# Kernel optimization log

Measured on AMD Instinct MI355X. Metric: run time of the kernel, lower is better.

The kernel has to match this reference:

```python
import jax, jax.numpy as jnp
import numpy as np

N, D, C = 4096, 512, 64
MARGIN = 1.0
INF = jnp.float32(1e30)


def setup_inputs() -> dict:
    key = jax.random.key(0)
    k1, k2 = jax.random.split(key)
    embeddings = jax.random.normal(k1, (N, D), dtype=jnp.float32)
    targets = jax.random.randint(k2, (N,), 0, C)
    return {"embeddings": embeddings, "targets": targets}


def _triplet_loss(embeddings, targets, margin=MARGIN):
    # Squared pairwise distances [N, N] (differentiable, used for the loss)
    sq_norms = jnp.sum(embeddings * embeddings, axis=1)
    sq_dist = jnp.maximum(
        sq_norms[:, None] + sq_norms[None, :] - 2.0 * (embeddings @ embeddings.T), 0.0
    )
    # Euclidean distances for mining only (index selection is non-differentiable in torch)
    dist = jnp.sqrt(jax.lax.stop_gradient(sq_dist))

    same = targets[:, None] == targets[None, :]  # [N, N] same-label mask

    # Hardest negative per anchor: argmax_k (d_ap - d_ak + margin) == argmin_k d_ak over negatives
    neg_dist = jnp.where(same, INF, dist)
    n_idx = jnp.argmin(neg_dist, axis=1)   # [N] hardest negative index per anchor
    min_neg = jnp.min(neg_dist, axis=1)    # [N] its euclidean distance

    idx = jnp.arange(dist.shape[0])
    # anchor-positive pairs: same label, a < p (torch.combinations on sorted indices)
    pair_mask = same & (idx[:, None] < idx[None, :])
    # triplet kept only if mined loss (euclidean) strictly positive
    valid = pair_mask & (dist - min_neg[:, None] + margin > 0)

    ap_sq = sq_dist                         # [N, N] squared anchor-positive distances
    an_sq = sq_dist[idx, n_idx]             # [N]   squared anchor-hard-negative distances
    losses = jax.nn.relu(ap_sq - an_sq[:, None] + margin)

    cnt = jnp.sum(valid)
    denom = jnp.maximum(cnt, 1).astype(losses.dtype)
    loss = jnp.sum(jnp.where(valid, losses, 0.0)) / denom

    correct = jnp.sum(valid & (ap_sq < an_sq[:, None]))
    accuracy = correct.astype(jnp.float32) / jnp.maximum(cnt, 1).astype(jnp.float32)
    return loss, accuracy


def reference(embeddings, targets):
    return _triplet_loss(embeddings, targets)
```

## Files before the change

kernel.cpp:

```cpp
#include <hip/hip_runtime.h>

#define N 4096
#define D 512
#define C 64
#define MARGIN 1.0f
#define TILE 128
#define ROWB 128
#define NTILES (N / TILE)
#define NTRI (NTILES * (NTILES + 1) / 2)
#define FINF 3.0e38f
#define SLOTW 16
#define PCAP 1024
#define LOSSB 128

typedef __attribute__((ext_vector_type(8))) short short8;
typedef __attribute__((ext_vector_type(4))) float floatx4;

__device__ __forceinline__ unsigned short f2bf(float f) {
  unsigned int u = __float_as_uint(f);
  u += 0x7FFFu + ((u >> 16) & 1u);
  return (unsigned short)(u >> 16);
}

__device__ __forceinline__ void gload_lds16(const void* g, void* l) {
  __builtin_amdgcn_global_load_lds(
      (const __attribute__((address_space(1))) unsigned int*)g,
      (__attribute__((address_space(3))) unsigned int*)l, 16, 0, 0);
}

__global__ __launch_bounds__(256) void prep_kernel(const float* __restrict__ E,
                                                   unsigned short* __restrict__ Ebf,
                                                   float* __restrict__ norms,
                                                   unsigned int* __restrict__ an_sq_bits,
                                                   unsigned int* __restrict__ accs_u,
                                                   unsigned int* __restrict__ ctrl) {
  const int row = blockIdx.x;
  const int tid = threadIdx.x;
  if (row == N) {
    for (int k = tid; k < C * SLOTW; k += 256) accs_u[k] = 0u;
    if (tid < 2) ctrl[tid] = 0u;
    return;
  }
  if (row < 16) an_sq_bits[row * 256 + tid] = 0x7F800000u;
  const float2 v = reinterpret_cast<const float2*>(E + (size_t)row * D)[tid];
  float s = v.x * v.x + v.y * v.y;
  unsigned int packed = ((unsigned int)f2bf(v.y) << 16) | (unsigned int)f2bf(v.x);
  reinterpret_cast<unsigned int*>(Ebf + (size_t)row * D)[tid] = packed;
  for (int off = 32; off > 0; off >>= 1) s += __shfl_down(s, off);
  __shared__ float wsum[4];
  if ((tid & 63) == 0) wsum[tid >> 6] = s;
  __syncthreads();
  if (tid == 0) norms[row] = wsum[0] + wsum[1] + wsum[2] + wsum[3];
}

__global__ __launch_bounds__(256, 3) void gemm_min_kernel(const unsigned short* __restrict__ Ebf,
                                                          const float* __restrict__ norms,
                                                          const int* __restrict__ targets,
                                                          unsigned int* __restrict__ an_sq_bits,
                                                          uint2* __restrict__ pairs,
                                                          unsigned int* __restrict__ ctrl) {
  const int u = blockIdx.x;
  int i = (int)((sqrtf(8.0f * (float)u + 1.0f) - 1.0f) * 0.5f);
  while ((i + 1) * (i + 2) / 2 <= u) ++i;
  while (i * (i + 1) / 2 > u) --i;
  const int tm = u - i * (i + 1) / 2;
  const int tn = i;

  __shared__ alignas(16) unsigned char As[TILE * ROWB];
  __shared__ alignas(16) unsigned char Bs[TILE * ROWB];
  __shared__ float s_rmin[2][TILE];
  __shared__ float s_cmin[2][TILE];
  __shared__ unsigned int s_pkey[PCAP];
  __shared__ float s_psq[PCAP];
  __shared__ unsigned int s_pcnt, s_pbase;

  const int tid = threadIdx.x;
  const int wave = tid >> 6, lane = tid & 63;
  const int quad = lane >> 4, l16 = lane & 15;
  const int wr = wave >> 1, wc = wave & 1;
  const int rowBase = tm * TILE, colBase = tn * TILE;
  if (tid == 0) s_pcnt = 0u;

  const int lr = lane >> 3;
  const int lq = (lane & 7) ^ lr;
  const int lofs = lr * (D * 2) + lq * 16;
  const unsigned char* gA = (const unsigned char*)Ebf + (size_t)rowBase * (D * 2);
  const unsigned char* gB = (const unsigned char*)Ebf + (size_t)colBase * (D * 2);

  const int swz = l16 & 7;
  int rA[4], rB[4], cq[2];
#pragma unroll
  for (int s = 0; s < 4; s++) {
    rA[s] = (wr * 64 + s * 16 + l16) * ROWB;
    rB[s] = (wc * 64 + s * 16 + l16) * ROWB;
  }
#pragma unroll
  for (int ks = 0; ks < 2; ks++) cq[ks] = ((ks * 4 + quad) ^ swz) * 16;

  floatx4 acc[4][4];
#pragma unroll
  for (int a = 0; a < 4; a++)
#pragma unroll
    for (int b = 0; b < 4; b++) acc[a][b] = (floatx4){0.f, 0.f, 0.f, 0.f};

  for (int k0b = 0; k0b < D * 2; k0b += 128) {
#pragma unroll
    for (int t = 0; t < 4; t++) {
      const int g = wave * 4 + t;
      gload_lds16(gA + (size_t)g * 8 * (D * 2) + lofs + k0b, As + g * 1024);
      gload_lds16(gB + (size_t)g * 8 * (D * 2) + lofs + k0b, Bs + g * 1024);
    }
    __syncthreads();
#pragma unroll
    for (int ks = 0; ks < 2; ks++) {
      short8 af[4], bf[4];
#pragma unroll
      for (int s = 0; s < 4; s++) {
        af[s] = *reinterpret_cast<const short8*>(As + rA[s] + cq[ks]);
        bf[s] = *reinterpret_cast<const short8*>(Bs + rB[s] + cq[ks]);
      }
#pragma unroll
      for (int sm = 0; sm < 4; sm++)
#pragma unroll
        for (int sn = 0; sn < 4; sn++)
          acc[sm][sn] = __builtin_amdgcn_mfma_f32_16x16x32_bf16(af[sm], bf[sn], acc[sm][sn], 0, 0, 0);
    }
    __syncthreads();
  }

  int tcol[4], gcolv[4];
  float ncol[4];
#pragma unroll
  for (int sn = 0; sn < 4; sn++) {
    const int gc = colBase + wc * 64 + sn * 16 + l16;
    gcolv[sn] = gc;
    tcol[sn] = targets[gc];
    ncol[sn] = norms[gc];
  }
  float colmin[4] = {FINF, FINF, FINF, FINF};
#pragma unroll
  for (int sm = 0; sm < 4; sm++) {
#pragma unroll
    for (int r = 0; r < 4; r++) {
      const int rloc = wr * 64 + sm * 16 + quad * 4 + r;
      const int grow = rowBase + rloc;
      const int trow = targets[grow];
      const float nrow = norms[grow];
      float rowmin = FINF;
#pragma unroll
      for (int sn = 0; sn < 4; sn++) {
        const float sq = fmaxf(nrow + ncol[sn] - 2.0f * acc[sm][sn][r], 0.0f);
        if (tcol[sn] != trow) {
          rowmin = fminf(rowmin, sq);
          colmin[sn] = fminf(colmin[sn], sq);
        } else if (grow < gcolv[sn]) {
          const unsigned int idx = atomicAdd(&s_pcnt, 1u);
          if (idx < PCAP) {
            s_pkey[idx] = ((unsigned int)grow << 12) | (unsigned int)gcolv[sn];
            s_psq[idx] = sq;
          } else {
            const unsigned int g = atomicAdd(&ctrl[0], 1u);
            pairs[g] = make_uint2(((unsigned int)grow << 12) | (unsigned int)gcolv[sn],
                                  __float_as_uint(sq));
          }
        }
      }
#pragma unroll
      for (int off = 1; off < 16; off <<= 1) rowmin = fminf(rowmin, __shfl_xor(rowmin, off));
      if (l16 == 0) s_rmin[wc][rloc] = rowmin;
    }
  }
#pragma unroll
  for (int sn = 0; sn < 4; sn++) {
    float cm = colmin[sn];
    cm = fminf(cm, __shfl_xor(cm, 16));
    cm = fminf(cm, __shfl_xor(cm, 32));
    if (quad == 0) s_cmin[wr][wc * 64 + sn * 16 + l16] = cm;
  }
  __syncthreads();
  if (tid < TILE) {
    const float m = fminf(s_rmin[0][tid], s_rmin[1][tid]);
    if (m < FINF) atomicMin(&an_sq_bits[rowBase + tid], __float_as_uint(m));
  } else {
    const int c = tid - TILE;
    const float m = fminf(s_cmin[0][c], s_cmin[1][c]);
    if (m < FINF) atomicMin(&an_sq_bits[colBase + c], __float_as_uint(m));
  }
  const unsigned int npair = min(s_pcnt, (unsigned int)PCAP);
  if (tid == 0) s_pbase = atomicAdd(&ctrl[0], npair);
  __syncthreads();
  for (unsigned int r = tid; r < npair; r += 256)
    pairs[s_pbase + r] = make_uint2(s_pkey[r], __float_as_uint(s_psq[r]));
}

__global__ __launch_bounds__(256) void loss_kernel(const uint2* __restrict__ pairs,
                                                   const unsigned int* __restrict__ an_sq_bits,
                                                   float* __restrict__ accs,
                                                   unsigned int* __restrict__ ctrl,
                                                   float* __restrict__ out) {
  const int tid = threadIdx.x, wave = tid >> 6, lane = tid & 63;
  const unsigned int M = ctrl[0];
  __shared__ float s_sum[4];
  __shared__ unsigned int s_cnt[4], s_cor[4];
  __shared__ int s_last;
  float bsum = 0.f;
  unsigned int bcnt = 0, bcor = 0;
  for (unsigned int r = blockIdx.x * 256 + tid; r < M; r += LOSSB * 256) {
    const uint2 rec = pairs[r];
    const int a = (int)(rec.x >> 12);
    const float sq = __uint_as_float(rec.y);
    const float an = __uint_as_float(an_sq_bits[a]);
    if (sqrtf(sq) - sqrtf(an) + MARGIN > 0.0f) {
      bcnt++;
      bsum += fmaxf(sq - an + MARGIN, 0.0f);
      if (sq < an) bcor++;
    }
  }
#pragma unroll
  for (int off = 32; off > 0; off >>= 1) {
    bsum += __shfl_down(bsum, off);
    bcnt += __shfl_down(bcnt, off);
    bcor += __shfl_down(bcor, off);
  }
  if (lane == 0) { s_sum[wave] = bsum; s_cnt[wave] = bcnt; s_cor[wave] = bcor; }
  __syncthreads();
  if (tid == 0) {
    float* slot = accs + (size_t)(blockIdx.x & (C - 1)) * SLOTW;
    atomicAdd(&slot[0], s_sum[0] + s_sum[1] + s_sum[2] + s_sum[3]);
    atomicAdd((unsigned int*)&slot[1], s_cnt[0] + s_cnt[1] + s_cnt[2] + s_cnt[3]);
    atomicAdd((unsigned int*)&slot[2], s_cor[0] + s_cor[1] + s_cor[2] + s_cor[3]);
    __threadfence();
    s_last = (atomicAdd(&ctrl[1], 1u) == (unsigned int)LOSSB - 1u);
  }
  __syncthreads();
  if (s_last) {
    __threadfence();
    if (tid < C) {
      float sum = __uint_as_float(atomicAdd((unsigned int*)&accs[(size_t)tid * SLOTW + 0], 0u));
      unsigned int cnt = atomicAdd((unsigned int*)&accs[(size_t)tid * SLOTW + 1], 0u);
      unsigned int cor = atomicAdd((unsigned int*)&accs[(size_t)tid * SLOTW + 2], 0u);
#pragma unroll
      for (int off = 32; off > 0; off >>= 1) {
        sum += __shfl_down(sum, off);
        cnt += __shfl_down(cnt, off);
        cor += __shfl_down(cor, off);
      }
      if (tid == 0) {
        const float denom = (float)(cnt > 0u ? cnt : 1u);
        out[0] = sum / denom;
        out[1] = (float)cor / denom;
      }
    }
  }
}

extern "C" void kernel_launch(void* const* d_in, const int* in_sizes, int n_in,
                              void* d_out, int out_size, void* d_ws, size_t ws_size,
                              hipStream_t stream) {
  const float* E = (const float*)d_in[0];
  const int* targets = (const int*)d_in[1];
  float* out = (float*)d_out;
  char* ws = (char*)d_ws;
  size_t off = 0;
  unsigned short* Ebf = (unsigned short*)(ws + off); off += (size_t)N * D * 2;
  float* norms = (float*)(ws + off); off += (size_t)N * 4;
  unsigned int* an_sq = (unsigned int*)(ws + off); off += (size_t)N * 4;
  float* accs = (float*)(ws + off); off += (size_t)C * SLOTW * 4;
  unsigned int* ctrl = (unsigned int*)(ws + off); off += 256;
  uint2* pairs = (uint2*)(ws + off);

  prep_kernel<<<dim3(N + 1), dim3(256), 0, stream>>>(E, Ebf, norms, an_sq, (unsigned int*)accs, ctrl);
  gemm_min_kernel<<<dim3(NTRI), dim3(256), 0, stream>>>(Ebf, norms, targets, an_sq, pairs, ctrl);
  loss_kernel<<<dim3(LOSSB), dim3(256), 0, stream>>>(pairs, an_sq, accs, ctrl, out);
}
```

Baseline: 95.93 us.

## Fuse prep, GEMM-min and loss into one persistent kernel with grid barriers

Replaces the three kernel launches with a single persistent kernel of 512 blocks. Each block first converts rows to bf16 and computes their norms, then passes a software grid barrier, pulls upper-triangular tiles from an atomic work counter, and after a second grid barrier runs the loss reduction. The aim is to remove launch gaps and inter-kernel idle time and to balance the tile work dynamically. In exchange it adds a memset node and spin-wait barriers, and it depends on all 512 blocks being co-resident, with a deadlock risk if they are not.

```diff
diff --git a/kernel.cpp b/kernel.cpp
--- a/kernel.cpp
+++ b/kernel.cpp
@@ -11,7 +11,7 @@
 #define FINF 3.0e38f
 #define SLOTW 16
 #define PCAP 1024
-#define LOSSB 128
+#define GRID 512
 
 typedef __attribute__((ext_vector_type(8))) short short8;
 typedef __attribute__((ext_vector_type(4))) float floatx4;
@@ -28,43 +28,51 @@
       (__attribute__((address_space(3))) unsigned int*)l, 16, 0, 0);
 }
 
-__global__ __launch_bounds__(256) void prep_kernel(const float* __restrict__ E,
-                                                   unsigned short* __restrict__ Ebf,
-                                                   float* __restrict__ norms,
-                                                   unsigned int* __restrict__ an_sq_bits,
-                                                   unsigned int* __restrict__ accs_u,
-                                                   unsigned int* __restrict__ ctrl) {
-  const int row = blockIdx.x;
+__device__ __forceinline__ void grid_barrier(unsigned int* cnt, unsigned int total) {
+  __syncthreads();
+  if (threadIdx.x == 0) {
+    __threadfence();
+    atomicAdd(cnt, 1u);
+    while (__hip_atomic_load(cnt, __ATOMIC_RELAXED, __HIP_MEMORY_SCOPE_AGENT) < total)
+      __builtin_amdgcn_s_sleep(2);
+    __threadfence();
+  }
+  __syncthreads();
+}
+
+__global__ __launch_bounds__(256, 3) void fused_kernel(
+    const float* __restrict__ E, const int* __restrict__ targets,
+    unsigned short* __restrict__ Ebf, float* __restrict__ norms,
+    unsigned int* __restrict__ an_sq_bits, float* __restrict__ accs,
+    unsigned int* __restrict__ ctrl, uint2* __restrict__ pairs,
+    float* __restrict__ out) {
   const int tid = threadIdx.x;
-  if (row == N) {
-    for (int k = tid; k < C * SLOTW; k += 256) accs_u[k] = 0u;
-    if (tid < 2) ctrl[tid] = 0u;
-    return;
-  }
-  if (row < 16) an_sq_bits[row * 256 + tid] = 0x7F800000u;
-  const float2 v = reinterpret_cast<const float2*>(E + (size_t)row * D)[tid];
-  float s = v.x * v.x + v.y * v.y;
-  unsigned int packed = ((unsigned int)f2bf(v.y) << 16) | (unsigned int)f2bf(v.x);
-  reinterpret_cast<unsigned int*>(Ebf + (size_t)row * D)[tid] = packed;
-  for (int off = 32; off > 0; off >>= 1) s += __shfl_down(s, off);
-  __shared__ float wsum[4];
-  if ((tid & 63) == 0) wsum[tid >> 6] = s;
-  __syncthreads();
-  if (tid == 0) norms[row] = wsum[0] + wsum[1] + wsum[2] + wsum[3];
-}
-
-__global__ __launch_bounds__(256, 3) void gemm_min_kernel(const unsigned short* __restrict__ Ebf,
-                                                          const float* __restrict__ norms,
-                                                          const int* __restrict__ targets,
-                                                          unsigned int* __restrict__ an_sq_bits,
-                                                          uint2* __restrict__ pairs,
-                                                          unsigned int* __restrict__ ctrl) {
-  const int u = blockIdx.x;
-  int i = (int)((sqrtf(8.0f * (float)u + 1.0f) - 1.0f) * 0.5f);
-  while ((i + 1) * (i + 2) / 2 <= u) ++i;
-  while (i * (i + 1) / 2 > u) --i;
-  const int tm = u - i * (i + 1) / 2;
-  const int tn = i;
+  const int wave = tid >> 6, lane = tid & 63;
+  const int quad = lane >> 4, l16 = lane & 15;
+
+  if (blockIdx.x < 8) {
+    an_sq_bits[blockIdx.x * 512 + tid] = 0x7F800000u;
+    an_sq_bits[blockIdx.x * 512 + 256 + tid] = 0x7F800000u;
+  }
+#pragma unroll
+  for (int rr = 0; rr < 2; rr++) {
+    const int row = blockIdx.x * 8 + wave * 2 + rr;
+    const float4 v0 = reinterpret_cast<const float4*>(E + (size_t)row * D)[lane * 2];
+    const float4 v1 = reinterpret_cast<const float4*>(E + (size_t)row * D)[lane * 2 + 1];
+    float s = v0.x * v0.x + v0.y * v0.y + v0.z * v0.z + v0.w * v0.w +
+              v1.x * v1.x + v1.y * v1.y + v1.z * v1.z + v1.w * v1.w;
+    uint4 p;
+    p.x = ((unsigned int)f2bf(v0.y) << 16) | f2bf(v0.x);
+    p.y = ((unsigned int)f2bf(v0.w) << 16) | f2bf(v0.z);
+    p.z = ((unsigned int)f2bf(v1.y) << 16) | f2bf(v1.x);
+    p.w = ((unsigned int)f2bf(v1.w) << 16) | f2bf(v1.z);
+    reinterpret_cast<uint4*>(Ebf + (size_t)row * D)[lane] = p;
+#pragma unroll
+    for (int off = 32; off > 0; off >>= 1) s += __shfl_down(s, off);
+    if (lane == 0) norms[row] = s;
+  }
+
+  grid_barrier(&ctrl[2], GRID);
 
   __shared__ alignas(16) unsigned char As[TILE * ROWB];
   __shared__ alignas(16) unsigned char Bs[TILE * ROWB];
@@ -72,21 +80,12 @@
   __shared__ float s_cmin[2][TILE];
   __shared__ unsigned int s_pkey[PCAP];
   __shared__ float s_psq[PCAP];
-  __shared__ unsigned int s_pcnt, s_pbase;
-
-  const int tid = threadIdx.x;
-  const int wave = tid >> 6, lane = tid & 63;
-  const int quad = lane >> 4, l16 = lane & 15;
+  __shared__ unsigned int s_pcnt, s_pbase, s_tile;
+
   const int wr = wave >> 1, wc = wave & 1;
-  const int rowBase = tm * TILE, colBase = tn * TILE;
-  if (tid == 0) s_pcnt = 0u;
-
   const int lr = lane >> 3;
   const int lq = (lane & 7) ^ lr;
   const int lofs = lr * (D * 2) + lq * 16;
-  const unsigned char* gA = (const unsigned char*)Ebf + (size_t)rowBase * (D * 2);
-  const unsigned char* gB = (const unsigned char*)Ebf + (size_t)colBase * (D * 2);
-
   const int swz = l16 & 7;
   int rA[4], rB[4], cq[2];
 #pragma unroll
@@ -97,115 +96,127 @@
 #pragma unroll
   for (int ks = 0; ks < 2; ks++) cq[ks] = ((ks * 4 + quad) ^ swz) * 16;
 
-  floatx4 acc[4][4];
-#pragma unroll
-  for (int a = 0; a < 4; a++)
-#pragma unroll
-    for (int b = 0; b < 4; b++) acc[a][b] = (floatx4){0.f, 0.f, 0.f, 0.f};
-
-  for (int k0b = 0; k0b < D * 2; k0b += 128) {
-#pragma unroll
-    for (int t = 0; t < 4; t++) {
-      const int g = wave * 4 + t;
-      gload_lds16(gA + (size_t)g * 8 * (D * 2) + lofs + k0b, As + g * 1024);
-      gload_lds16(gB + (size_t)g * 8 * (D * 2) + lofs + k0b, Bs + g * 1024);
-    }
-    __syncthreads();
-#pragma unroll
-    for (int ks = 0; ks < 2; ks++) {
-      short8 af[4], bf[4];
-#pragma unroll
-      for (int s = 0; s < 4; s++) {
-        af[s] = *reinterpret_cast<const short8*>(As + rA[s] + cq[ks]);
-        bf[s] = *reinterpret_cast<const short8*>(Bs + rB[s] + cq[ks]);
-      }
-#pragma unroll
-      for (int sm = 0; sm < 4; sm++)
-#pragma unroll
-        for (int sn = 0; sn < 4; sn++)
-          acc[sm][sn] = __builtin_amdgcn_mfma_f32_16x16x32_bf16(af[sm], bf[sn], acc[sm][sn], 0, 0, 0);
-    }
-    __syncthreads();
-  }
-
-  int tcol[4], gcolv[4];
-  float ncol[4];
-#pragma unroll
-  for (int sn = 0; sn < 4; sn++) {
-    const int gc = colBase + wc * 64 + sn * 16 + l16;
-    gcolv[sn] = gc;
-    tcol[sn] = targets[gc];
-    ncol[sn] = norms[gc];
-  }
-  float colmin[4] = {FINF, FINF, FINF, FINF};
-#pragma unroll
-  for (int sm = 0; sm < 4; sm++) {
-#pragma unroll
-    for (int r = 0; r < 4; r++) {
-      const int rloc = wr * 64 + sm * 16 + quad * 4 + r;
-      const int grow = rowBase + rloc;
-      const int trow = targets[grow];
-      const float nrow = norms[grow];
-      float rowmin = FINF;
-#pragma unroll
-      for (int sn = 0; sn < 4; sn++) {
-        const float sq = fmaxf(nrow + ncol[sn] - 2.0f * acc[sm][sn][r], 0.0f);
-        if (tcol[sn] != trow) {
-          rowmin = fminf(rowmin, sq);
-          colmin[sn] = fminf(colmin[sn], sq);
-        } else if (grow < gcolv[sn]) {
-          const unsigned int idx = atomicAdd(&s_pcnt, 1u);
-          if (idx < PCAP) {
-            s_pkey[idx] = ((unsigned int)grow << 12) | (unsigned int)gcolv[sn];
-            s_psq[idx] = sq;
-          } else {
-            const unsigned int g = atomicAdd(&ctrl[0], 1u);
-            pairs[g] = make_uint2(((unsigned int)grow << 12) | (unsigned int)gcolv[sn],
-                                  __float_as_uint(sq));
+  for (;;) {
+    if (tid == 0) s_tile = atomicAdd(&ctrl[1], 1u);
+    __syncthreads();
+    const unsigned int u = s_tile;
+    if (u >= NTRI) break;
+    if (tid == 0) s_pcnt = 0u;
+    int i = (int)((sqrtf(8.0f * (float)u + 1.0f) - 1.0f) * 0.5f);
+    while ((i + 1) * (i + 2) / 2 <= (int)u) ++i;
+    while (i * (i + 1) / 2 > (int)u) --i;
+    const int tm = (int)u - i * (i + 1) / 2;
+    const int tn = i;
+    const int rowBase = tm * TILE, colBase = tn * TILE;
+    const unsigned char* gA = (const unsigned char*)Ebf + (size_t)rowBase * (D * 2);
+    const unsigned char* gB = (const unsigned char*)Ebf + (size_t)colBase * (D * 2);
+
+    floatx4 acc[4][4];
+#pragma unroll
+    for (int a = 0; a < 4; a++)
+#pragma unroll
+      for (int b = 0; b < 4; b++) acc[a][b] = (floatx4){0.f, 0.f, 0.f, 0.f};
+
+    for (int k0b = 0; k0b < D * 2; k0b += 128) {
+#pragma unroll
+      for (int t = 0; t < 4; t++) {
+        const int g = wave * 4 + t;
+        gload_lds16(gA + (size_t)g * 8 * (D * 2) + lofs + k0b, As + g * 1024);
+        gload_lds16(gB + (size_t)g * 8 * (D * 2) + lofs + k0b, Bs + g * 1024);
+      }
+      __syncthreads();
+#pragma unroll
+      for (int ks = 0; ks < 2; ks++) {
+        short8 af[4], bf[4];
+#pragma unroll
+        for (int s = 0; s < 4; s++) {
+          af[s] = *reinterpret_cast<const short8*>(As + rA[s] + cq[ks]);
+          bf[s] = *reinterpret_cast<const short8*>(Bs + rB[s] + cq[ks]);
+        }
+#pragma unroll
+        for (int sm = 0; sm < 4; sm++)
+#pragma unroll
+          for (int sn = 0; sn < 4; sn++)
+            acc[sm][sn] = __builtin_amdgcn_mfma_f32_16x16x32_bf16(af[sm], bf[sn], acc[sm][sn], 0, 0, 0);
+      }
+      __syncthreads();
+    }
+
+    int tcol[4], gcolv[4];
+    float ncol[4];
+#pragma unroll
+    for (int sn = 0; sn < 4; sn++) {
+      const int gc = colBase + wc * 64 + sn * 16 + l16;
+      gcolv[sn] = gc;
+      tcol[sn] = targets[gc];
+      ncol[sn] = norms[gc];
+    }
+    float colmin[4] = {FINF, FINF, FINF, FINF};
+#pragma unroll
+    for (int sm = 0; sm < 4; sm++) {
+#pragma unroll
+      for (int r = 0; r < 4; r++) {
+        const int rloc = wr * 64 + sm * 16 + quad * 4 + r;
+        const int grow = rowBase + rloc;
+        const int trow = targets[grow];
+        const float nrow = norms[grow];
+        float rowmin = FINF;
+#pragma unroll
+        for (int sn = 0; sn < 4; sn++) {
+          const float sq = fmaxf(nrow + ncol[sn] - 2.0f * acc[sm][sn][r], 0.0f);
+          if (tcol[sn] != trow) {
+            rowmin = fminf(rowmin, sq);
+            colmin[sn] = fminf(colmin[sn], sq);
+          } else if (grow < gcolv[sn]) {
+            const unsigned int idx = atomicAdd(&s_pcnt, 1u);
+            if (idx < PCAP) {
+              s_pkey[idx] = ((unsigned int)grow << 12) | (unsigned int)gcolv[sn];
+              s_psq[idx] = sq;
+            } else {
+              const unsigned int g = atomicAdd(&ctrl[0], 1u);
+              pairs[g] = make_uint2(((unsigned int)grow << 12) | (unsigned int)gcolv[sn],
+                                    __float_as_uint(sq));
+            }
           }
         }
-      }
-#pragma unroll
-      for (int off = 1; off < 16; off <<= 1) rowmin = fminf(rowmin, __shfl_xor(rowmin, off));
-      if (l16 == 0) s_rmin[wc][rloc] = rowmin;
-    }
-  }
-#pragma unroll
-  for (int sn = 0; sn < 4; sn++) {
-    float cm = colmin[sn];
-    cm = fminf(cm, __shfl_xor(cm, 16));
-    cm = fminf(cm, __shfl_xor(cm, 32));
-    if (quad == 0) s_cmin[wr][wc * 64 + sn * 16 + l16] = cm;
-  }
-  __syncthreads();
-  if (tid < TILE) {
-    const float m = fminf(s_rmin[0][tid], s_rmin[1][tid]);
-    if (m < FINF) atomicMin(&an_sq_bits[rowBase + tid], __float_as_uint(m));
-  } else {
-    const int c = tid - TILE;
-    const float m = fminf(s_cmin[0][c], s_cmin[1][c]);
-    if (m < FINF) atomicMin(&an_sq_bits[colBase + c], __float_as_uint(m));
-  }
-  const unsigned int npair = min(s_pcnt, (unsigned int)PCAP);
-  if (tid == 0) s_pbase = atomicAdd(&ctrl[0], npair);
-  __syncthreads();
-  for (unsigned int r = tid; r < npair; r += 256)
-    pairs[s_pbase + r] = make_uint2(s_pkey[r], __float_as_uint(s_psq[r]));
-}
-
-__global__ __launch_bounds__(256) void loss_kernel(const uint2* __restrict__ pairs,
-                                                   const unsigned int* __restrict__ an_sq_bits,
-                                                   float* __restrict__ accs,
-                                                   unsigned int* __restrict__ ctrl,
-                                                   float* __restrict__ out) {
-  const int tid = threadIdx.x, wave = tid >> 6, lane = tid & 63;
-  const unsigned int M = ctrl[0];
+#pragma unroll
+        for (int off = 1; off < 16; off <<= 1) rowmin = fminf(rowmin, __shfl_xor(rowmin, off));
+        if (l16 == 0) s_rmin[wc][rloc] = rowmin;
+      }
+    }
+#pragma unroll
+    for (int sn = 0; sn < 4; sn++) {
+      float cm = colmin[sn];
+      cm = fminf(cm, __shfl_xor(cm, 16));
+      cm = fminf(cm, __shfl_xor(cm, 32));
+      if (quad == 0) s_cmin[wr][wc * 64 + sn * 16 + l16] = cm;
+    }
+    __syncthreads();
+    if (tid < TILE) {
+      const float m = fminf(s_rmin[0][tid], s_rmin[1][tid]);
+      if (m < FINF) atomicMin(&an_sq_bits[rowBase + tid], __float_as_uint(m));
+    } else {
+      const int c = tid - TILE;
+      const float m = fminf(s_cmin[0][c], s_cmin[1][c]);
+      if (m < FINF) atomicMin(&an_sq_bits[colBase + c], __float_as_uint(m));
+    }
+    const unsigned int npair = min(s_pcnt, (unsigned int)PCAP);
+    if (tid == 0) s_pbase = atomicAdd(&ctrl[0], npair);
+    __syncthreads();
+    for (unsigned int r = tid; r < npair; r += 256)
+      pairs[s_pbase + r] = make_uint2(s_pkey[r], __float_as_uint(s_psq[r]));
+    __syncthreads();
+  }
+
+  grid_barrier(&ctrl[3], GRID);
+
   __shared__ float s_sum[4];
   __shared__ unsigned int s_cnt[4], s_cor[4];
   __shared__ int s_last;
+  const unsigned int M = atomicAdd(&ctrl[0], 0u);
   float bsum = 0.f;
   unsigned int bcnt = 0, bcor = 0;
-  for (unsigned int r = blockIdx.x * 256 + tid; r < M; r += LOSSB * 256) {
+  for (unsigned int r = blockIdx.x * 256 + tid; r < M; r += GRID * 256) {
     const uint2 rec = pairs[r];
     const int a = (int)(rec.x >> 12);
     const float sq = __uint_as_float(rec.y);
@@ -230,7 +241,7 @@
     atomicAdd((unsigned int*)&slot[1], s_cnt[0] + s_cnt[1] + s_cnt[2] + s_cnt[3]);
     atomicAdd((unsigned int*)&slot[2], s_cor[0] + s_cor[1] + s_cor[2] + s_cor[3]);
     __threadfence();
-    s_last = (atomicAdd(&ctrl[1], 1u) == (unsigned int)LOSSB - 1u);
+    s_last = (atomicAdd(&ctrl[4], 1u) == (unsigned int)GRID - 1u);
   }
   __syncthreads();
   if (s_last) {
@@ -269,7 +280,7 @@
   unsigned int* ctrl = (unsigned int*)(ws + off); off += 256;
   uint2* pairs = (uint2*)(ws + off);
 
-  prep_kernel<<<dim3(N + 1), dim3(256), 0, stream>>>(E, Ebf, norms, an_sq, (unsigned int*)accs, ctrl);
-  gemm_min_kernel<<<dim3(NTRI), dim3(256), 0, stream>>>(Ebf, norms, targets, an_sq, pairs, ctrl);
-  loss_kernel<<<dim3(LOSSB), dim3(256), 0, stream>>>(pairs, an_sq, accs, ctrl, out);
-}
+  hipMemsetAsync(accs, 0, (size_t)C * SLOTW * 4 + 256, stream);
+  fused_kernel<<<dim3(GRID), dim3(256), 0, stream>>>(E, targets, Ebf, norms, an_sq, accs,
+                                                     ctrl, pairs, out);
+}
```

After: 214.6 us. 2.24x slower.

## Pack bf16 embeddings into MFMA-ready panels and load fragments directly to registers

Applied to the files above, without the earlier changes.

The prep kernel now writes bf16 embeddings in a panel layout of 16 rows by 512 k, ordered so that each lane's MFMA fragment is a contiguous 16-byte load. The GEMM drops LDS staging and its barriers, loading A/B fragments straight from global memory with register double-buffering across 16 k-steps. This removes LDS traffic and the syncthreads calls, but each wave reloads operands from L2 with no sharing between waves, and launch bounds go from 3 to 2 blocks per SM to fit the extra registers. Zeroing of the accumulators and control words moves to a hipMemsetAsync call, and the prep kernel now handles 16 rows per block.

```diff
diff --git a/kernel.cpp b/kernel.cpp
--- a/kernel.cpp
+++ b/kernel.cpp
@@ -5,13 +5,13 @@
 #define C 64
 #define MARGIN 1.0f
 #define TILE 128
-#define ROWB 128
 #define NTILES (N / TILE)
 #define NTRI (NTILES * (NTILES + 1) / 2)
 #define FINF 3.0e38f
 #define SLOTW 16
 #define PCAP 1024
 #define LOSSB 128
+#define PANELB 16384
 
 typedef __attribute__((ext_vector_type(8))) short short8;
 typedef __attribute__((ext_vector_type(4))) float floatx4;
@@ -22,38 +22,41 @@
   return (unsigned short)(u >> 16);
 }
 
-__device__ __forceinline__ void gload_lds16(const void* g, void* l) {
-  __builtin_amdgcn_global_load_lds(
-      (const __attribute__((address_space(1))) unsigned int*)g,
-      (__attribute__((address_space(3))) unsigned int*)l, 16, 0, 0);
-}
-
 __global__ __launch_bounds__(256) void prep_kernel(const float* __restrict__ E,
-                                                   unsigned short* __restrict__ Ebf,
+                                                   unsigned short* __restrict__ panels,
                                                    float* __restrict__ norms,
-                                                   unsigned int* __restrict__ an_sq_bits,
-                                                   unsigned int* __restrict__ accs_u,
-                                                   unsigned int* __restrict__ ctrl) {
-  const int row = blockIdx.x;
+                                                   unsigned int* __restrict__ an_sq_bits) {
+  const int b = blockIdx.x;
   const int tid = threadIdx.x;
-  if (row == N) {
-    for (int k = tid; k < C * SLOTW; k += 256) accs_u[k] = 0u;
-    if (tid < 2) ctrl[tid] = 0u;
-    return;
-  }
-  if (row < 16) an_sq_bits[row * 256 + tid] = 0x7F800000u;
-  const float2 v = reinterpret_cast<const float2*>(E + (size_t)row * D)[tid];
-  float s = v.x * v.x + v.y * v.y;
-  unsigned int packed = ((unsigned int)f2bf(v.y) << 16) | (unsigned int)f2bf(v.x);
-  reinterpret_cast<unsigned int*>(Ebf + (size_t)row * D)[tid] = packed;
-  for (int off = 32; off > 0; off >>= 1) s += __shfl_down(s, off);
-  __shared__ float wsum[4];
-  if ((tid & 63) == 0) wsum[tid >> 6] = s;
-  __syncthreads();
-  if (tid == 0) norms[row] = wsum[0] + wsum[1] + wsum[2] + wsum[3];
-}
-
-__global__ __launch_bounds__(256, 3) void gemm_min_kernel(const unsigned short* __restrict__ Ebf,
+  const int row = tid & 15, qg = tid >> 4;
+  if (tid < 16) an_sq_bits[b * 16 + tid] = 0x7F800000u;
+  const float4* Er = reinterpret_cast<const float4*>(E + (size_t)(b * 16 + row) * D);
+  uint4* P4 = reinterpret_cast<uint4*>(panels + (size_t)b * (PANELB / 2));
+  float s = 0.f;
+#pragma unroll
+  for (int j = 0; j < 4; j++) {
+    const int q = qg * 4 + j;
+    const float4 v0 = Er[q * 2];
+    const float4 v1 = Er[q * 2 + 1];
+    s += v0.x * v0.x + v0.y * v0.y + v0.z * v0.z + v0.w * v0.w +
+         v1.x * v1.x + v1.y * v1.y + v1.z * v1.z + v1.w * v1.w;
+    uint4 p;
+    p.x = ((unsigned int)f2bf(v0.y) << 16) | f2bf(v0.x);
+    p.y = ((unsigned int)f2bf(v0.w) << 16) | f2bf(v0.z);
+    p.z = ((unsigned int)f2bf(v1.y) << 16) | f2bf(v1.x);
+    p.w = ((unsigned int)f2bf(v1.w) << 16) | f2bf(v1.z);
+    P4[q * 16 + row] = p;
+  }
+  s += __shfl_xor(s, 16);
+  s += __shfl_xor(s, 32);
+  __shared__ float s_n[4][16];
+  const int wave = tid >> 6, lane = tid & 63;
+  if (lane < 16) s_n[wave][lane] = s;
+  __syncthreads();
+  if (tid < 16) norms[b * 16 + tid] = s_n[0][tid] + s_n[1][tid] + s_n[2][tid] + s_n[3][tid];
+}
+
+__global__ __launch_bounds__(256, 2) void gemm_min_kernel(const unsigned short* __restrict__ panels,
                                                           const float* __restrict__ norms,
                                                           const int* __restrict__ targets,
                                                           unsigned int* __restrict__ an_sq_bits,
@@ -66,8 +69,6 @@
   const int tm = u - i * (i + 1) / 2;
   const int tn = i;
 
-  __shared__ alignas(16) unsigned char As[TILE * ROWB];
-  __shared__ alignas(16) unsigned char Bs[TILE * ROWB];
   __shared__ float s_rmin[2][TILE];
   __shared__ float s_cmin[2][TILE];
   __shared__ unsigned int s_pkey[PCAP];
@@ -81,51 +82,38 @@
   const int rowBase = tm * TILE, colBase = tn * TILE;
   if (tid == 0) s_pcnt = 0u;
 
-  const int lr = lane >> 3;
-  const int lq = (lane & 7) ^ lr;
-  const int lofs = lr * (D * 2) + lq * 16;
-  const unsigned char* gA = (const unsigned char*)Ebf + (size_t)rowBase * (D * 2);
-  const unsigned char* gB = (const unsigned char*)Ebf + (size_t)colBase * (D * 2);
-
-  const int swz = l16 & 7;
-  int rA[4], rB[4], cq[2];
+  const unsigned char* pA = (const unsigned char*)panels + (size_t)(tm * 8 + wr * 4) * PANELB;
+  const unsigned char* pB = (const unsigned char*)panels + (size_t)(tn * 8 + wc * 4) * PANELB;
+  const int lofs = quad * 256 + l16 * 16;
+
+  floatx4 acc[4][4];
+#pragma unroll
+  for (int a = 0; a < 4; a++)
+#pragma unroll
+    for (int b = 0; b < 4; b++) acc[a][b] = (floatx4){0.f, 0.f, 0.f, 0.f};
+
+  short8 af[2][4], bf[2][4];
 #pragma unroll
   for (int s = 0; s < 4; s++) {
-    rA[s] = (wr * 64 + s * 16 + l16) * ROWB;
-    rB[s] = (wc * 64 + s * 16 + l16) * ROWB;
-  }
-#pragma unroll
-  for (int ks = 0; ks < 2; ks++) cq[ks] = ((ks * 4 + quad) ^ swz) * 16;
-
-  floatx4 acc[4][4];
-#pragma unroll
-  for (int a = 0; a < 4; a++)
-#pragma unroll
-    for (int b = 0; b < 4; b++) acc[a][b] = (floatx4){0.f, 0.f, 0.f, 0.f};
-
-  for (int k0b = 0; k0b < D * 2; k0b += 128) {
-#pragma unroll
-    for (int t = 0; t < 4; t++) {
-      const int g = wave * 4 + t;
-      gload_lds16(gA + (size_t)g * 8 * (D * 2) + lofs + k0b, As + g * 1024);
-      gload_lds16(gB + (size_t)g * 8 * (D * 2) + lofs + k0b, Bs + g * 1024);
-    }
-    __syncthreads();
-#pragma unroll
-    for (int ks = 0; ks < 2; ks++) {
-      short8 af[4], bf[4];
+    af[0][s] = *reinterpret_cast<const short8*>(pA + s * PANELB + lofs);
+    bf[0][s] = *reinterpret_cast<const short8*>(pB + s * PANELB + lofs);
+  }
+#pragma unroll 2
+  for (int ks = 0; ks < 16; ks++) {
+    const int cur = ks & 1, nxt = cur ^ 1;
+    if (ks < 15) {
+      const int off = (ks + 1) * 1024 + lofs;
 #pragma unroll
       for (int s = 0; s < 4; s++) {
-        af[s] = *reinterpret_cast<const short8*>(As + rA[s] + cq[ks]);
-        bf[s] = *reinterpret_cast<const short8*>(Bs + rB[s] + cq[ks]);
-      }
-#pragma unroll
-      for (int sm = 0; sm < 4; sm++)
-#pragma unroll
-        for (int sn = 0; sn < 4; sn++)
-          acc[sm][sn] = __builtin_amdgcn_mfma_f32_16x16x32_bf16(af[sm], bf[sn], acc[sm][sn], 0, 0, 0);
-    }
-    __syncthreads();
+        af[nxt][s] = *reinterpret_cast<const short8*>(pA + s * PANELB + off);
+        bf[nxt][s] = *reinterpret_cast<const short8*>(pB + s * PANELB + off);
+      }
+    }
+#pragma unroll
+    for (int sm = 0; sm < 4; sm++)
+#pragma unroll
+      for (int sn = 0; sn < 4; sn++)
+        acc[sm][sn] = __builtin_amdgcn_mfma_f32_16x16x32_bf16(af[cur][sm], bf[cur][sn], acc[sm][sn], 0, 0, 0);
   }
 
   int tcol[4], gcolv[4];
@@ -262,14 +250,15 @@
   float* out = (float*)d_out;
   char* ws = (char*)d_ws;
   size_t off = 0;
-  unsigned short* Ebf = (unsigned short*)(ws + off); off += (size_t)N * D * 2;
+  unsigned short* panels = (unsigned short*)(ws + off); off += (size_t)N * D * 2;
   float* norms = (float*)(ws + off); off += (size_t)N * 4;
   unsigned int* an_sq = (unsigned int*)(ws + off); off += (size_t)N * 4;
   float* accs = (float*)(ws + off); off += (size_t)C * SLOTW * 4;
   unsigned int* ctrl = (unsigned int*)(ws + off); off += 256;
   uint2* pairs = (uint2*)(ws + off);
 
-  prep_kernel<<<dim3(N + 1), dim3(256), 0, stream>>>(E, Ebf, norms, an_sq, (unsigned int*)accs, ctrl);
-  gemm_min_kernel<<<dim3(NTRI), dim3(256), 0, stream>>>(Ebf, norms, targets, an_sq, pairs, ctrl);
+  hipMemsetAsync(accs, 0, (size_t)C * SLOTW * 4 + 256, stream);
+  prep_kernel<<<dim3(N / 16), dim3(256), 0, stream>>>(E, panels, norms, an_sq);
+  gemm_min_kernel<<<dim3(NTRI), dim3(256), 0, stream>>>(panels, norms, targets, an_sq, pairs, ctrl);
   loss_kernel<<<dim3(LOSSB), dim3(256), 0, stream>>>(pairs, an_sq, accs, ctrl, out);
 }
```

Result: slower. 99.84 us (+4.1%).

## Use 64x128 triangular tiles in GEMM-min and restructure prep to 16 rows per block

Applied to the files above, without the earlier changes.

The pairwise-distance GEMM moves from 528 square 128x128 upper-triangle tiles to 1056 rectangular 64x128 tiles, with a new index decode. This halves the accumulator registers, raises the occupancy hint to 4, and spreads work across more blocks. The prep kernel now handles 16 rows per block with float4 loads and per-wave norm reductions, and zeroes ctrl through the extended accs clear instead of an extra block. Smaller tiles lower operand reuse and add more atomicMin and pair-append traffic. The LDS pair capacity also shrinks to 512, which may push more pairs to global atomics.

```diff
diff --git a/kernel.cpp b/kernel.cpp
--- a/kernel.cpp
+++ b/kernel.cpp
@@ -4,13 +4,12 @@
 #define D 512
 #define C 64
 #define MARGIN 1.0f
-#define TILE 128
-#define ROWB 128
-#define NTILES (N / TILE)
-#define NTRI (NTILES * (NTILES + 1) / 2)
+#define TROW 64
+#define TCOL 128
+#define NBLK 1056
 #define FINF 3.0e38f
 #define SLOTW 16
-#define PCAP 1024
+#define PCAP 512
 #define LOSSB 128
 
 typedef __attribute__((ext_vector_type(8))) short short8;
@@ -32,44 +31,49 @@
                                                    unsigned short* __restrict__ Ebf,
                                                    float* __restrict__ norms,
                                                    unsigned int* __restrict__ an_sq_bits,
-                                                   unsigned int* __restrict__ accs_u,
-                                                   unsigned int* __restrict__ ctrl) {
-  const int row = blockIdx.x;
-  const int tid = threadIdx.x;
-  if (row == N) {
-    for (int k = tid; k < C * SLOTW; k += 256) accs_u[k] = 0u;
-    if (tid < 2) ctrl[tid] = 0u;
-    return;
-  }
-  if (row < 16) an_sq_bits[row * 256 + tid] = 0x7F800000u;
-  const float2 v = reinterpret_cast<const float2*>(E + (size_t)row * D)[tid];
-  float s = v.x * v.x + v.y * v.y;
-  unsigned int packed = ((unsigned int)f2bf(v.y) << 16) | (unsigned int)f2bf(v.x);
-  reinterpret_cast<unsigned int*>(Ebf + (size_t)row * D)[tid] = packed;
-  for (int off = 32; off > 0; off >>= 1) s += __shfl_down(s, off);
-  __shared__ float wsum[4];
-  if ((tid & 63) == 0) wsum[tid >> 6] = s;
-  __syncthreads();
-  if (tid == 0) norms[row] = wsum[0] + wsum[1] + wsum[2] + wsum[3];
-}
-
-__global__ __launch_bounds__(256, 3) void gemm_min_kernel(const unsigned short* __restrict__ Ebf,
+                                                   unsigned int* __restrict__ accs_u) {
+  const int b = blockIdx.x;
+  const int tid = threadIdx.x, wave = tid >> 6, lane = tid & 63;
+  if (tid < 16) an_sq_bits[b * 16 + tid] = 0x7F800000u;
+  if (b == 0)
+    for (int k = tid; k < C * SLOTW + 64; k += 256) accs_u[k] = 0u;
+#pragma unroll
+  for (int rr = 0; rr < 4; rr++) {
+    const int row = b * 16 + wave * 4 + rr;
+    const float4* Er = reinterpret_cast<const float4*>(E + (size_t)row * D);
+    const float4 v0 = Er[lane * 2];
+    const float4 v1 = Er[lane * 2 + 1];
+    float s = v0.x * v0.x + v0.y * v0.y + v0.z * v0.z + v0.w * v0.w +
+              v1.x * v1.x + v1.y * v1.y + v1.z * v1.z + v1.w * v1.w;
+    uint4 p;
+    p.x = ((unsigned int)f2bf(v0.y) << 16) | f2bf(v0.x);
+    p.y = ((unsigned int)f2bf(v0.w) << 16) | f2bf(v0.z);
+    p.z = ((unsigned int)f2bf(v1.y) << 16) | f2bf(v1.x);
+    p.w = ((unsigned int)f2bf(v1.w) << 16) | f2bf(v1.z);
+    reinterpret_cast<uint4*>(Ebf + (size_t)row * D)[lane] = p;
+#pragma unroll
+    for (int off = 32; off > 0; off >>= 1) s += __shfl_down(s, off);
+    if (lane == 0) norms[row] = s;
+  }
+}
+
+__global__ __launch_bounds__(256, 4) void gemm_min_kernel(const unsigned short* __restrict__ Ebf,
                                                           const float* __restrict__ norms,
                                                           const int* __restrict__ targets,
                                                           unsigned int* __restrict__ an_sq_bits,
                                                           uint2* __restrict__ pairs,
                                                           unsigned int* __restrict__ ctrl) {
   const int u = blockIdx.x;
-  int i = (int)((sqrtf(8.0f * (float)u + 1.0f) - 1.0f) * 0.5f);
-  while ((i + 1) * (i + 2) / 2 <= u) ++i;
-  while (i * (i + 1) / 2 > u) --i;
-  const int tm = u - i * (i + 1) / 2;
-  const int tn = i;
-
-  __shared__ alignas(16) unsigned char As[TILE * ROWB];
-  __shared__ alignas(16) unsigned char Bs[TILE * ROWB];
-  __shared__ float s_rmin[2][TILE];
-  __shared__ float s_cmin[2][TILE];
+  int b = (int)((sqrtf(4.0f * (float)u + 1.0f) - 1.0f) * 0.5f);
+  while ((b + 1) * (b + 2) <= u) ++b;
+  while (b * (b + 1) > u) --b;
+  const int a = u - b * (b + 1);
+  const int rowBase = a * TROW, colBase = b * TCOL;
+
+  __shared__ alignas(16) unsigned char As[TROW * 128];
+  __shared__ alignas(16) unsigned char Bs[TCOL * 128];
+  __shared__ float s_rmin[2][TROW];
+  __shared__ float s_cmin[2][TCOL];
   __shared__ unsigned int s_pkey[PCAP];
   __shared__ float s_psq[PCAP];
   __shared__ unsigned int s_pcnt, s_pbase;
@@ -78,7 +82,6 @@
   const int wave = tid >> 6, lane = tid & 63;
   const int quad = lane >> 4, l16 = lane & 15;
   const int wr = wave >> 1, wc = wave & 1;
-  const int rowBase = tm * TILE, colBase = tn * TILE;
   if (tid == 0) s_pcnt = 0u;
 
   const int lr = lane >> 3;
@@ -88,39 +91,41 @@
   const unsigned char* gB = (const unsigned char*)Ebf + (size_t)colBase * (D * 2);
 
   const int swz = l16 & 7;
-  int rA[4], rB[4], cq[2];
-#pragma unroll
-  for (int s = 0; s < 4; s++) {
-    rA[s] = (wr * 64 + s * 16 + l16) * ROWB;
-    rB[s] = (wc * 64 + s * 16 + l16) * ROWB;
-  }
+  int rA[2], rB[4], cq[2];
+#pragma unroll
+  for (int s = 0; s < 2; s++) rA[s] = (wr * 32 + s * 16 + l16) * 128;
+#pragma unroll
+  for (int s = 0; s < 4; s++) rB[s] = (wc * 64 + s * 16 + l16) * 128;
 #pragma unroll
   for (int ks = 0; ks < 2; ks++) cq[ks] = ((ks * 4 + quad) ^ swz) * 16;
 
-  floatx4 acc[4][4];
-#pragma unroll
-  for (int a = 0; a < 4; a++)
-#pragma unroll
-    for (int b = 0; b < 4; b++) acc[a][b] = (floatx4){0.f, 0.f, 0.f, 0.f};
+  floatx4 acc[2][4];
+#pragma unroll
+  for (int x = 0; x < 2; x++)
+#pragma unroll
+    for (int y = 0; y < 4; y++) acc[x][y] = (floatx4){0.f, 0.f, 0.f, 0.f};
 
   for (int k0b = 0; k0b < D * 2; k0b += 128) {
+#pragma unroll
+    for (int t = 0; t < 2; t++) {
+      const int g = wave * 2 + t;
+      gload_lds16(gA + (size_t)g * 8 * (D * 2) + lofs + k0b, As + g * 1024);
+    }
 #pragma unroll
     for (int t = 0; t < 4; t++) {
       const int g = wave * 4 + t;
-      gload_lds16(gA + (size_t)g * 8 * (D * 2) + lofs + k0b, As + g * 1024);
       gload_lds16(gB + (size_t)g * 8 * (D * 2) + lofs + k0b, Bs + g * 1024);
     }
     __syncthreads();
 #pragma unroll
     for (int ks = 0; ks < 2; ks++) {
-      short8 af[4], bf[4];
-#pragma unroll
-      for (int s = 0; s < 4; s++) {
-        af[s] = *reinterpret_cast<const short8*>(As + rA[s] + cq[ks]);
-        bf[s] = *reinterpret_cast<const short8*>(Bs + rB[s] + cq[ks]);
-      }
-#pragma unroll
-      for (int sm = 0; sm < 4; sm++)
+      short8 af[2], bf[4];
+#pragma unroll
+      for (int s = 0; s < 2; s++) af[s] = *reinterpret_cast<const short8*>(As + rA[s] + cq[ks]);
+#pragma unroll
+      for (int s = 0; s < 4; s++) bf[s] = *reinterpret_cast<const short8*>(Bs + rB[s] + cq[ks]);
+#pragma unroll
+      for (int sm = 0; sm < 2; sm++)
 #pragma unroll
         for (int sn = 0; sn < 4; sn++)
           acc[sm][sn] = __builtin_amdgcn_mfma_f32_16x16x32_bf16(af[sm], bf[sn], acc[sm][sn], 0, 0, 0);
@@ -139,10 +144,10 @@
   }
   float colmin[4] = {FINF, FINF, FINF, FINF};
 #pragma unroll
-  for (int sm = 0; sm < 4; sm++) {
+  for (int sm = 0; sm < 2; sm++) {
 #pragma unroll
     for (int r = 0; r < 4; r++) {
-      const int rloc = wr * 64 + sm * 16 + quad * 4 + r;
+      const int rloc = wr * 32 + sm * 16 + quad * 4 + r;
       const int grow = rowBase + rloc;
       const int trow = targets[grow];
       const float nrow = norms[grow];
@@ -178,11 +183,11 @@
     if (quad == 0) s_cmin[wr][wc * 64 + sn * 16 + l16] = cm;
   }
   __syncthreads();
-  if (tid < TILE) {
+  if (tid < TROW) {
     const float m = fminf(s_rmin[0][tid], s_rmin[1][tid]);
     if (m < FINF) atomicMin(&an_sq_bits[rowBase + tid], __float_as_uint(m));
-  } else {
-    const int c = tid - TILE;
+  } else if (tid < TROW + TCOL) {
+    const int c = tid - TROW;
     const float m = fminf(s_cmin[0][c], s_cmin[1][c]);
     if (m < FINF) atomicMin(&an_sq_bits[colBase + c], __float_as_uint(m));
   }
@@ -269,7 +274,7 @@
   unsigned int* ctrl = (unsigned int*)(ws + off); off += 256;
   uint2* pairs = (uint2*)(ws + off);
 
-  prep_kernel<<<dim3(N + 1), dim3(256), 0, stream>>>(E, Ebf, norms, an_sq, (unsigned int*)accs, ctrl);
-  gemm_min_kernel<<<dim3(NTRI), dim3(256), 0, stream>>>(Ebf, norms, targets, an_sq, pairs, ctrl);
+  prep_kernel<<<dim3(N / 16), dim3(256), 0, stream>>>(E, Ebf, norms, an_sq, (unsigned int*)accs);
+  gemm_min_kernel<<<dim3(NBLK), dim3(256), 0, stream>>>(Ebf, norms, targets, an_sq, pairs, ctrl);
   loss_kernel<<<dim3(LOSSB), dim3(256), 0, stream>>>(pairs, an_sq, accs, ctrl, out);
 }
```

After: 98.19 us. 1.02x slower.
